# Optimization experiments

Measured on AMD Instinct MI355X. Metric: run time of the kernel, lower is better.

The kernel has to match this reference:

```python
import jax, jax.numpy as jnp
import numpy as np

B, S, D = 2, 2048, 4096
H, KVH, HD = 32, 8, 128
WIN = 1024  # sliding window
THETA = 10000.0


def setup_inputs() -> dict:
    key = jax.random.key(0)
    ks = jax.random.split(key, 5)
    x = jax.random.normal(ks[0], (B, S, D), jnp.float32) * 0.02
    wq = jax.random.normal(ks[1], (H * HD, D), jnp.float32) * 0.02
    wk = jax.random.normal(ks[2], (KVH * HD, D), jnp.float32) * 0.02
    wv = jax.random.normal(ks[3], (KVH * HD, D), jnp.float32) * 0.02
    wo = jax.random.normal(ks[4], (D, H * HD), jnp.float32) * 0.02
    positions = jnp.arange(S, dtype=jnp.int32)
    inv_freq = 1.0 / (THETA ** (jnp.arange(0, HD, 2, dtype=jnp.float32) / HD))
    ang = positions.astype(jnp.float32)[:, None] * inv_freq[None, :]  # [S, HD/2]
    cos, sin = jnp.cos(ang), jnp.sin(ang)
    i = jnp.arange(S)[:, None]
    j = jnp.arange(S)[None, :]
    allowed = (j <= i) & (i - j < WIN)  # causal + sliding window
    mask = jnp.where(allowed, 0.0, -1e9).astype(jnp.float32)  # [S, S]
    return {"x": x, "wq": wq, "wk": wk, "wv": wv, "wo": wo,
            "cos": cos, "sin": sin, "mask": mask, "positions": positions}


def _apply_rope(t, cos, sin):
    # t: [B, S, nH, HD]; pairs are consecutive dims (torch view_as_complex layout)
    tr = t.reshape(t.shape[:-1] + (HD // 2, 2))
    t0, t1 = tr[..., 0], tr[..., 1]
    c = cos[None, :, None, :]
    s = sin[None, :, None, :]
    out = jnp.stack([t0 * c - t1 * s, t0 * s + t1 * c], axis=-1)
    return out.reshape(t.shape)


def reference(x, wq, wk, wv, wo, cos, sin, mask, positions):
    bsz, seqlen, _ = x.shape
    xq = (x @ wq.T).reshape(bsz, seqlen, H, HD)
    xk = (x @ wk.T).reshape(bsz, seqlen, KVH, HD)
    xv = (x @ wv.T).reshape(bsz, seqlen, KVH, HD)
    xq = _apply_rope(xq, cos, sin)
    xk = _apply_rope(xk, cos, sin)
    # GQA: repeat_kv head broadcast (prefill path: positions.size(0) > 1)
    rep = H // KVH
    key = jnp.repeat(xk, rep, axis=2)  # [B, S, H, HD]
    val = jnp.repeat(xv, rep, axis=2)
    q = xq.transpose(0, 2, 1, 3)  # [B, H, S, HD]
    k = key.transpose(0, 2, 1, 3)
    v = val.transpose(0, 2, 1, 3)
    scale = HD ** -0.5
    scores = jnp.einsum("bhqd,bhkd->bhqk", q, k) * scale
    scores = scores + mask[None, None, :, :]
    probs = jax.nn.softmax(scores.astype(jnp.float32), axis=-1).astype(q.dtype)
    out = jnp.einsum("bhqk,bhkd->bhqd", probs, v)
    out = out.transpose(0, 2, 1, 3).reshape(bsz, seqlen, H * HD)
    return out @ wo.T
```

## Files before the change

kernel.cpp:

```cpp
#include <hip/hip_runtime.h>
#include <hip/hip_bf16.h>

#define B_  2
#define S_  2048
#define D_  4096
#define H_  32
#define KVH_ 8
#define HD_ 128
#define WIN_ 1024
#define KVSTR 2048

typedef __attribute__((ext_vector_type(8))) __bf16 bf16x8;
typedef __attribute__((ext_vector_type(4))) float f32x4;
using bf16 = __hip_bfloat16;

typedef const __attribute__((address_space(1))) void* gas_ptr;
typedef __attribute__((address_space(3))) void* las_ptr;

__device__ __forceinline__ void gload16(const void* g, void* l) {
    __builtin_amdgcn_global_load_lds((gas_ptr)g, (las_ptr)l, 16, 0, 0);
}

__device__ __forceinline__ bf16x8 load8(const bf16* p) {
    return *reinterpret_cast<const bf16x8*>(p);
}
__device__ __forceinline__ bf16x8 cvt8(const bf16* p) {
    return *reinterpret_cast<const bf16x8*>(p);
}
__device__ __forceinline__ bf16x8 cvt8(const float* p) {
    const float4* q = reinterpret_cast<const float4*>(p);
    float4 a = q[0], b = q[1];
    bf16x8 r;
    r[0] = (__bf16)a.x; r[1] = (__bf16)a.y; r[2] = (__bf16)a.z; r[3] = (__bf16)a.w;
    r[4] = (__bf16)b.x; r[5] = (__bf16)b.y; r[6] = (__bf16)b.z; r[7] = (__bf16)b.w;
    return r;
}
__device__ __forceinline__ void store1(float* p, float v) { *p = v; }
__device__ __forceinline__ void store1(bf16* p, float v) { *p = __float2bfloat16(v); }

#define GBAR()  __builtin_amdgcn_s_barrier()
#define SCB0()  __builtin_amdgcn_sched_barrier(0)
#define LGKM0() do { asm volatile("s_waitcnt lgkmcnt(0)" ::: "memory"); \
                     __builtin_amdgcn_sched_barrier(0); } while (0)
#define VMC(n)  do { asm volatile("s_waitcnt vmcnt(" #n ")" ::: "memory"); \
                     __builtin_amdgcn_sched_barrier(0); } while (0)

__global__ __launch_bounds__(256) void cast_kernel(const float* __restrict__ in,
                                                   bf16* __restrict__ out) {
    long i = ((long)blockIdx.x * 256 + threadIdx.x) * 8;
    const float4* p = reinterpret_cast<const float4*>(in + i);
    float4 a = p[0], b = p[1];
    bf16x8 r;
    r[0] = (__bf16)a.x; r[1] = (__bf16)a.y; r[2] = (__bf16)a.z; r[3] = (__bf16)a.w;
    r[4] = (__bf16)b.x; r[5] = (__bf16)b.y; r[6] = (__bf16)b.z; r[7] = (__bf16)b.w;
    *reinterpret_cast<bf16x8*>(out + i) = r;
}

__global__ __launch_bounds__(256) void cast2_kernel(
    const float* __restrict__ in0, bf16* __restrict__ out0,
    const float* __restrict__ in1, bf16* __restrict__ out1, int n0blocks) {
    const bool first = (int)blockIdx.x < n0blocks;
    const float* in = first ? in0 : in1;
    bf16* out = first ? out0 : out1;
    long bid = first ? blockIdx.x : (blockIdx.x - n0blocks);
    long i = (bid * 256 + threadIdx.x) * 8;
    const float4* p = reinterpret_cast<const float4*>(in + i);
    float4 a = p[0], b = p[1];
    bf16x8 r;
    r[0] = (__bf16)a.x; r[1] = (__bf16)a.y; r[2] = (__bf16)a.z; r[3] = (__bf16)a.w;
    r[4] = (__bf16)b.x; r[5] = (__bf16)b.y; r[6] = (__bf16)b.z; r[7] = (__bf16)b.w;
    *reinterpret_cast<bf16x8*>(out + i) = r;
}

__device__ __forceinline__ void xcd_swizzle(int& bx, int& by, int nbx, int nby) {
    int flat = bx + nbx * by;
    int nwg  = nbx * nby;
    int cpx  = nwg >> 3;
    int swz  = (flat & 7) * cpx + (flat >> 3);
    bx = swz % nbx;
    by = swz / nbx;
}

template <typename TC>
__global__ __launch_bounds__(512, 2) void gemm_nt_256(
    const bf16* __restrict__ A, const bf16* __restrict__ Bm,
    TC* __restrict__ C, int M, int N, int K) {
    __shared__ __bf16 lds[2][2][256 * 64];

    const int tid  = threadIdx.x;
    const int wave = tid >> 6;
    const int lane = tid & 63;
    const int col  = lane & 15;
    const int quad = lane >> 4;
    const int c7   = col & 7;
    const int wmi  = wave >> 2;
    const int wni  = wave & 3;
    int bx = blockIdx.x, by = blockIdx.y;
    xcd_swizzle(bx, by, gridDim.x, gridDim.y);
    const long m0  = (long)by * 256;
    const long n0  = (long)bx * 256;
    const int  nt  = K >> 6;

    f32x4 zero = {0.f, 0.f, 0.f, 0.f};
    f32x4 acc[8][4];
#pragma unroll
    for (int i = 0; i < 8; i++)
#pragma unroll
        for (int j = 0; j < 4; j++) acc[i][j] = zero;

    long gA[4], gB[4];
    int  lofs[4];
#pragma unroll
    for (int j = 0; j < 4; j++) {
        int r  = j * 64 + wave * 8 + (lane >> 3);
        int cg = (lane & 7) ^ (r & 7);
        gA[j]   = (m0 + r) * (long)K + cg * 8;
        gB[j]   = (n0 + r) * (long)K + cg * 8;
        lofs[j] = (j * 64 + wave * 8) * 128;
    }

#pragma unroll
    for (int j = 0; j < 4; j++) {
        gload16(A  + gA[j], (char*)lds[0][0] + lofs[j]);
        gload16(Bm + gB[j], (char*)lds[0][1] + lofs[j]);
    }
    if (nt > 1) {
#pragma unroll
        for (int j = 0; j < 4; j++)
            gload16(Bm + gB[j] + 64, (char*)lds[1][1] + lofs[j]);
        gload16(A + gA[0] + 64, (char*)lds[1][0] + lofs[0]);
        gload16(A + gA[2] + 64, (char*)lds[1][0] + lofs[2]);
        VMC(6);
    } else {
        VMC(0);
    }
    GBAR();

#define RDA_(dst, mf, ks) \
    dst = *reinterpret_cast<const bf16x8*>(Ab + (wmi * 128 + (mf) * 16 + col) * 128 \
                                              + ((((ks) << 2) + quad) ^ c7) * 16)
#define MFMA16(mb) \
    do { \
        _Pragma("unroll") \
        for (int ks = 0; ks < 2; ks++) { \
            _Pragma("unroll") \
            for (int nf = 0; nf < 4; nf++) { \
                acc[mb][nf]     = __builtin_amdgcn_mfma_f32_16x16x32_bf16( \
                    a[0][ks], bfr[nf][ks], acc[mb][nf], 0, 0, 0); \
                acc[mb + 1][nf] = __builtin_amdgcn_mfma_f32_16x16x32_bf16( \
                    a[1][ks], bfr[nf][ks], acc[mb + 1][nf], 0, 0, 0); \
            } \
        } \
    } while (0)

    for (int t = 0; t < nt; ++t) {
        const int cur = t & 1;
        const char* Ab = (const char*)lds[cur][0];
        const char* Bb = (const char*)lds[cur][1];
        char* An2 = (char*)lds[cur ^ 1][0];
        char* Ac2 = (char*)lds[cur][0];
        char* Bc2 = (char*)lds[cur][1];

        bf16x8 bfr[4][2];
#pragma unroll
        for (int nf = 0; nf < 4; nf++)
#pragma unroll
            for (int ks = 0; ks < 2; ks++)
                bfr[nf][ks] = *reinterpret_cast<const bf16x8*>(
                    Bb + (wni * 64 + nf * 16 + col) * 128 + (((ks << 2) + quad) ^ c7) * 16);
        bf16x8 a[2][2];
        RDA_(a[0][0], 0, 0); RDA_(a[0][1], 0, 1);
        RDA_(a[1][0], 1, 0); RDA_(a[1][1], 1, 1);
        if (t + 1 < nt) {
            long ko = (long)(t + 1) * 64;
            gload16(A + gA[1] + ko, An2 + lofs[1]);
            gload16(A + gA[3] + ko, An2 + lofs[3]);
        }
        GBAR();
        LGKM0();
        __builtin_amdgcn_s_setprio(1);
        MFMA16(0);
        __builtin_amdgcn_s_setprio(0);
        GBAR();

        RDA_(a[0][0], 2, 0); RDA_(a[0][1], 2, 1);
        RDA_(a[1][0], 3, 0); RDA_(a[1][1], 3, 1);
        if (t + 2 < nt) {
            long ko = (long)(t + 2) * 64;
#pragma unroll
            for (int j = 0; j < 4; j++)
                gload16(Bm + gB[j] + ko, Bc2 + lofs[j]);
        }
        GBAR();
        LGKM0();
        __builtin_amdgcn_s_setprio(1);
        MFMA16(2);
        __builtin_amdgcn_s_setprio(0);
        GBAR();

        RDA_(a[0][0], 4, 0); RDA_(a[0][1], 4, 1);
        RDA_(a[1][0], 5, 0); RDA_(a[1][1], 5, 1);
        if (t + 2 < nt) {
            long ko = (long)(t + 2) * 64;
            gload16(A + gA[0] + ko, Ac2 + lofs[0]);
            gload16(A + gA[2] + ko, Ac2 + lofs[2]);
        }
        GBAR();
        LGKM0();
        __builtin_amdgcn_s_setprio(1);
        MFMA16(4);
        __builtin_amdgcn_s_setprio(0);
        GBAR();

        RDA_(a[0][0], 6, 0); RDA_(a[0][1], 6, 1);
        RDA_(a[1][0], 7, 0); RDA_(a[1][1], 7, 1);
        LGKM0();
        __builtin_amdgcn_s_setprio(1);
        MFMA16(6);
        __builtin_amdgcn_s_setprio(0);
        if (t + 2 < nt) { VMC(6); } else { VMC(0); }
        GBAR();
    }

#pragma unroll
    for (int mf = 0; mf < 8; mf++) {
#pragma unroll
        for (int nf = 0; nf < 4; nf++) {
            long row = m0 + wmi * 128 + mf * 16 + quad * 4;
            long cc  = n0 + wni * 64 + nf * 16 + col;
#pragma unroll
            for (int r = 0; r < 4; r++)
                store1(&C[(row + r) * (long)N + cc], acc[mf][nf][r]);
        }
    }
}

template <typename TC>
__global__ __launch_bounds__(256) void gemm_nt_fast(
    const bf16* __restrict__ A, const bf16* __restrict__ Bm,
    TC* __restrict__ C, int M, int N, int K) {
    __shared__ __bf16 As[128 * 64];
    __shared__ __bf16 Bs[128 * 64];

    const int tid  = threadIdx.x;
    const int wave = tid >> 6;
    const int lane = tid & 63;
    const int col  = lane & 15;
    const int quad = lane >> 4;
    const int c7   = col & 7;
    const int wm   = (wave >> 1) * 64;
    const int wn   = (wave & 1) * 64;
    int bx = blockIdx.x, by = blockIdx.y;
    xcd_swizzle(bx, by, gridDim.x, gridDim.y);
    const long m0  = (long)by * 128;
    const long n0  = (long)bx * 128;

    f32x4 zero = {0.f, 0.f, 0.f, 0.f};
    f32x4 acc[4][4];
#pragma unroll
    for (int i = 0; i < 4; i++)
#pragma unroll
        for (int j = 0; j < 4; j++) acc[i][j] = zero;

    long goffA[4], goffB[4];
    int  loff[4];
#pragma unroll
    for (int i = 0; i < 4; i++) {
        int r  = (wave * 4 + i) * 8 + (lane >> 3);
        int cg = (lane & 7) ^ (r & 7);
        goffA[i] = (m0 + r) * (long)K + cg * 8;
        goffB[i] = (n0 + r) * (long)K + cg * 8;
        loff[i]  = (wave * 4 + i) * 1024;
    }

    for (int kt = 0; kt < K; kt += 64) {
#pragma unroll
        for (int i = 0; i < 4; i++) {
            gload16(A + goffA[i] + kt, (char*)As + loff[i]);
            gload16(Bm + goffB[i] + kt, (char*)Bs + loff[i]);
        }
        __syncthreads();

        bf16x8 af[2][4], bfv[2][4];
#pragma unroll
        for (int ks = 0; ks < 2; ks++) {
#pragma unroll
            for (int mt = 0; mt < 4; mt++) {
                int row = wm + mt * 16 + col;
                af[ks][mt] = *reinterpret_cast<const bf16x8*>(
                    (const char*)As + row * 128 + (((ks << 2) + quad) ^ c7) * 16);
            }
#pragma unroll
            for (int nt = 0; nt < 4; nt++) {
                int row = wn + nt * 16 + col;
                bfv[ks][nt] = *reinterpret_cast<const bf16x8*>(
                    (const char*)Bs + row * 128 + (((ks << 2) + quad) ^ c7) * 16);
            }
        }
#pragma unroll
        for (int ks = 0; ks < 2; ks++)
#pragma unroll
            for (int mt = 0; mt < 4; mt++)
#pragma unroll
                for (int nt = 0; nt < 4; nt++)
                    acc[mt][nt] = __builtin_amdgcn_mfma_f32_16x16x32_bf16(
                        af[ks][mt], bfv[ks][nt], acc[mt][nt], 0, 0, 0);
        __syncthreads();
    }

#pragma unroll
    for (int mt = 0; mt < 4; mt++) {
#pragma unroll
        for (int nt = 0; nt < 4; nt++) {
            long row = m0 + wm + mt * 16 + quad * 4;
            long cc  = n0 + wn + nt * 16 + col;
#pragma unroll
            for (int r = 0; r < 4; r++)
                store1(&C[(row + r) * (long)N + cc], acc[mt][nt][r]);
        }
    }
}

template <typename TA, typename TB, typename TC>
__global__ __launch_bounds__(256) void gemm_nt(
    const TA* __restrict__ A, const TB* __restrict__ Bm,
    TC* __restrict__ C, int M, int N, int K, int ldc) {
    __shared__ __bf16 As[128 * 40];
    __shared__ __bf16 Bs[128 * 40];

    const int tid  = threadIdx.x;
    const int wave = tid >> 6;
    const int lane = tid & 63;
    const int col  = lane & 15;
    const int quad = lane >> 4;
    const int wm   = (wave >> 1) * 64;
    const int wn   = (wave & 1) * 64;
    const long m0  = (long)blockIdx.y * 128;
    const long n0  = (long)blockIdx.x * 128;

    f32x4 zero = {0.f, 0.f, 0.f, 0.f};
    f32x4 acc[4][4];
#pragma unroll
    for (int i = 0; i < 4; i++)
#pragma unroll
        for (int j = 0; j < 4; j++) acc[i][j] = zero;

    const int srow = tid >> 2;
    const int sch  = (tid & 3) * 8;

    for (int kt = 0; kt < K; kt += 32) {
        bf16x8 av0 = cvt8(A + (m0 + srow)      * (long)K + kt + sch);
        bf16x8 av1 = cvt8(A + (m0 + srow + 64) * (long)K + kt + sch);
        bf16x8 bv0 = cvt8(Bm + (n0 + srow)      * (long)K + kt + sch);
        bf16x8 bv1 = cvt8(Bm + (n0 + srow + 64) * (long)K + kt + sch);
        *reinterpret_cast<bf16x8*>(&As[srow * 40 + sch])        = av0;
        *reinterpret_cast<bf16x8*>(&As[(srow + 64) * 40 + sch]) = av1;
        *reinterpret_cast<bf16x8*>(&Bs[srow * 40 + sch])        = bv0;
        *reinterpret_cast<bf16x8*>(&Bs[(srow + 64) * 40 + sch]) = bv1;
        __syncthreads();

        bf16x8 af[4], bfv[4];
#pragma unroll
        for (int mt = 0; mt < 4; mt++)
            af[mt] = *reinterpret_cast<const bf16x8*>(&As[(wm + mt * 16 + col) * 40 + quad * 8]);
#pragma unroll
        for (int nt = 0; nt < 4; nt++)
            bfv[nt] = *reinterpret_cast<const bf16x8*>(&Bs[(wn + nt * 16 + col) * 40 + quad * 8]);
#pragma unroll
        for (int mt = 0; mt < 4; mt++)
#pragma unroll
            for (int nt = 0; nt < 4; nt++)
                acc[mt][nt] = __builtin_amdgcn_mfma_f32_16x16x32_bf16(
                    af[mt], bfv[nt], acc[mt][nt], 0, 0, 0);
        __syncthreads();
    }

#pragma unroll
    for (int mt = 0; mt < 4; mt++) {
#pragma unroll
        for (int nt = 0; nt < 4; nt++) {
            long row = m0 + wm + mt * 16 + quad * 4;
            long cc  = n0 + wn + nt * 16 + col;
#pragma unroll
            for (int r = 0; r < 4; r++)
                store1(&C[(row + r) * (long)ldc + cc], acc[mt][nt][r]);
        }
    }
}

__global__ __launch_bounds__(256) void rope2_kernel(
    bf16* __restrict__ qb, bf16* __restrict__ kvb,
    const float* __restrict__ cosb, const float* __restrict__ sinb) {
    const int NQ = B_ * S_ * H_ * 64;
    int idx = blockIdx.x * 256 + threadIdx.x;
    bf16* t; int nh, stride;
    if (idx < NQ) { t = qb;  nh = H_;   stride = H_ * HD_; }
    else          { t = kvb; nh = KVH_; stride = KVSTR; idx -= NQ; }
    int pair = idx & 63;
    int rest = idx >> 6;
    int hh   = rest % nh;
    int tok  = rest / nh;
    int s    = tok & (S_ - 1);
    long base = (long)tok * stride + hh * HD_ + pair * 2;
    float c  = cosb[s * 64 + pair];
    float sn = sinb[s * 64 + pair];
    float t0 = __bfloat162float(t[base]);
    float t1 = __bfloat162float(t[base + 1]);
    t[base]     = __float2bfloat16(t0 * c - t1 * sn);
    t[base + 1] = __float2bfloat16(t0 * sn + t1 * c);
}

__global__ __launch_bounds__(256) void transpose_v(const bf16* __restrict__ kv,
                                                   bf16* __restrict__ vt) {
    __shared__ __bf16 tile[64][72];
    const int s0 = blockIdx.x * 64;
    const int d0 = blockIdx.y * 64;
    const int b  = blockIdx.z;
    const int tid = threadIdx.x;
    const int tr  = tid >> 3;
    const int c8  = (tid & 7) * 8;
#pragma unroll
    for (int p = 0; p < 2; p++) {
        int srow = tr + p * 32;
        bf16x8 val = load8(kv + ((long)(b * S_ + s0 + srow)) * KVSTR + 1024 + d0 + c8);
        *reinterpret_cast<bf16x8*>(&tile[srow][c8]) = val;
    }
    __syncthreads();
#pragma unroll
    for (int p = 0; p < 2; p++) {
        int dd = tr + p * 32;
        bf16x8 ov;
#pragma unroll
        for (int j = 0; j < 8; j++) ov[j] = tile[c8 + j][dd];
        *reinterpret_cast<bf16x8*>(vt + ((long)(b * 1024 + d0 + dd)) * S_ + s0 + c8) = ov;
    }
}

__global__ __launch_bounds__(512, 4) void attn_kernel(
    const bf16* __restrict__ q, const bf16* __restrict__ kv,
    const bf16* __restrict__ vt, bf16* __restrict__ o) {
    const int qb  = blockIdx.x;
    const int hp  = blockIdx.y;
    const int b   = blockIdx.z;
    const int tid = threadIdx.x;
    const int wave = tid >> 6;
    const int lane = tid & 63;
    const int col  = lane & 15;
    const int quad = lane >> 4;
    const int h    = hp * 2 + (wave >> 2);
    const int wq4  = wave & 3;
    const int kvh  = hp >> 1;
    const int i0   = qb * 64;
    const float scale = 0.08838834764831845f;

    __shared__ __bf16 Ks[64 * 128];
    __shared__ __bf16 Vs[128 * 64];
    __shared__ __bf16 Pl[8][16 * 72];

    bf16x8 qa[4];
    const bf16* qptr = q + ((long)(b * S_ + i0 + wq4 * 16 + col)) * (H_ * HD_)
                         + h * HD_ + quad * 8;
#pragma unroll
    for (int ks = 0; ks < 4; ks++) qa[ks] = load8(qptr + ks * 32);

    long gK[2], gV[2];
    int  lK[2], lV[2];
#pragma unroll
    for (int i = 0; i < 2; i++) {
        int ck  = wave * 2 + i;
        int rK  = ck * 4 + (lane >> 4);
        int cgK = (lane & 15) ^ (rK & 15);
        gK[i] = ((long)(b * S_) + rK) * KVSTR + kvh * HD_ + cgK * 8;
        lK[i] = ck * 1024;
        int rV  = ck * 8 + (lane >> 3);
        int cgV = (lane & 7) ^ (rV & 7);
        gV[i] = ((long)(b * 1024) + kvh * HD_ + rV) * (long)S_ + cgV * 8;
        lV[i] = ck * 1024;
    }

    f32x4 zero = {0.f, 0.f, 0.f, 0.f};
    f32x4 oacc[8];
#pragma unroll
    for (int i = 0; i < 8; i++) oacc[i] = zero;
    float lsum[4] = {0.f, 0.f, 0.f, 0.f};

    const int kb0 = (qb >= 16) ? (qb - 16) : 0;

    bf16x8 kreg[2], vreg[2];
#pragma unroll
    for (int i = 0; i < 2; i++) {
        kreg[i] = *reinterpret_cast<const bf16x8*>(kv + gK[i] + (long)kb0 * 64 * KVSTR);
        vreg[i] = *reinterpret_cast<const bf16x8*>(vt + gV[i] + kb0 * 64);
    }

    for (int kb = kb0; kb <= qb; kb++) {
        GBAR();
        SCB0();
#pragma unroll
        for (int i = 0; i < 2; i++) {
            *reinterpret_cast<bf16x8*>((char*)Ks + lK[i] + lane * 16) = kreg[i];
            *reinterpret_cast<bf16x8*>((char*)Vs + lV[i] + lane * 16) = vreg[i];
        }
        LGKM0();
        GBAR();
        SCB0();
        if (kb < qb) {
#pragma unroll
            for (int i = 0; i < 2; i++) {
                kreg[i] = *reinterpret_cast<const bf16x8*>(
                    kv + gK[i] + (long)(kb + 1) * 64 * KVSTR);
                vreg[i] = *reinterpret_cast<const bf16x8*>(
                    vt + gV[i] + (kb + 1) * 64);
            }
            SCB0();
        }

        f32x4 sfr[4];
        __builtin_amdgcn_s_setprio(1);
#pragma unroll
        for (int nt = 0; nt < 4; nt++) {
            f32x4 s = zero;
            int row = nt * 16 + col;
#pragma unroll
            for (int ks = 0; ks < 4; ks++) {
                bf16x8 bfv = *reinterpret_cast<const bf16x8*>(
                    (const char*)Ks + row * 256 + (((ks << 2) + quad) ^ col) * 16);
                s = __builtin_amdgcn_mfma_f32_16x16x32_bf16(qa[ks], bfv, s, 0, 0, 0);
            }
            sfr[nt] = s;
        }
        __builtin_amdgcn_s_setprio(0);
#pragma unroll
        for (int nt = 0; nt < 4; nt++) {
            int j = kb * 64 + nt * 16 + col;
#pragma unroll
            for (int r = 0; r < 4; r++) {
                int i = i0 + wq4 * 16 + quad * 4 + r;
                float p = 0.f;
                if (j <= i && (i - j) < WIN_) p = __expf(sfr[nt][r] * scale);
                lsum[r] += p;
                Pl[wave][(quad * 4 + r) * 72 + nt * 16 + col] = __float2bfloat16(p);
            }
        }
        __builtin_amdgcn_s_setprio(1);
#pragma unroll
        for (int ks2 = 0; ks2 < 2; ks2++) {
            bf16x8 pa = *reinterpret_cast<const bf16x8*>(
                &Pl[wave][col * 72 + ks2 * 32 + quad * 8]);
#pragma unroll
            for (int nt2 = 0; nt2 < 8; nt2++) {
                int d = nt2 * 16 + col;
                bf16x8 vb = *reinterpret_cast<const bf16x8*>(
                    (const char*)Vs + d * 128 + ((((ks2 << 2) + quad)) ^ (col & 7)) * 16);
                oacc[nt2] = __builtin_amdgcn_mfma_f32_16x16x32_bf16(
                    pa, vb, oacc[nt2], 0, 0, 0);
            }
        }
        __builtin_amdgcn_s_setprio(0);
    }

#pragma unroll
    for (int m = 1; m < 16; m <<= 1) {
#pragma unroll
        for (int r = 0; r < 4; r++) lsum[r] += __shfl_xor(lsum[r], m, 64);
    }

    bf16* op = o + ((long)(b * S_ + i0 + wq4 * 16 + quad * 4)) * (H_ * HD_) + h * HD_;
#pragma unroll
    for (int nt2 = 0; nt2 < 8; nt2++) {
#pragma unroll
        for (int r = 0; r < 4; r++)
            op[(long)r * (H_ * HD_) + nt2 * 16 + col] =
                __float2bfloat16(oacc[nt2][r] / lsum[r]);
    }
}

extern "C" void kernel_launch(void* const* d_in, const int* in_sizes, int n_in,
                              void* d_out, int out_size, void* d_ws, size_t ws_size,
                              hipStream_t stream) {
    const float* x    = (const float*)d_in[0];
    const float* wq   = (const float*)d_in[1];
    const float* wk   = (const float*)d_in[2];
    const float* wv   = (const float*)d_in[3];
    const float* wo   = (const float*)d_in[4];
    const float* cosb = (const float*)d_in[5];
    const float* sinb = (const float*)d_in[6];
    float* out = (float*)d_out;

    const size_t T   = (size_t)B_ * S_;
    const size_t SZ_D  = T * (H_ * HD_);
    const size_t SZ_KV = T * (KVH_ * HD_);

    dim3 blk(256);
    const size_t need_fast = (SZ_D * 3 + SZ_KV * 3 + SZ_D) * 2;

    if (ws_size >= need_fast) {
        bf16* xb    = (bf16*)d_ws;
        bf16* wbuf  = xb    + SZ_D;
        bf16* q_ws  = wbuf  + SZ_D;
        bf16* kv_ws = q_ws  + SZ_D;
        bf16* vt_ws = kv_ws + 2 * SZ_KV;
        bf16* ao_ws = vt_ws + SZ_KV;

        cast2_kernel<<<2 * (SZ_D / 2048), blk, 0, stream>>>(x, xb, wq, wbuf,
                                                            (int)(SZ_D / 2048));
        gemm_nt_256<bf16><<<dim3(16, 16), dim3(512), 0, stream>>>(xb, wbuf, q_ws, 4096, 4096, 4096);

        cast2_kernel<<<2 * (SZ_KV / 2048), blk, 0, stream>>>(wk, wbuf, wv, wbuf + SZ_KV,
                                                             (int)(SZ_KV / 2048));
        gemm_nt_fast<bf16><<<dim3(16, 32), blk, 0, stream>>>(xb, wbuf, kv_ws, 4096, 2048, 4096);

        rope2_kernel<<<(B_ * S_ * (H_ + KVH_) * 64) / 256, blk, 0, stream>>>(
            q_ws, kv_ws, cosb, sinb);
        transpose_v<<<dim3(32, 16, 2), blk, 0, stream>>>(kv_ws, vt_ws);

        attn_kernel<<<dim3(32, 16, 2), dim3(512), 0, stream>>>(q_ws, kv_ws, vt_ws, ao_ws);

        cast_kernel<<<SZ_D / 2048, blk, 0, stream>>>(wo, wbuf);
        gemm_nt_256<float><<<dim3(16, 16), dim3(512), 0, stream>>>(ao_ws, wbuf, out, 4096, 4096, 4096);
    } else {
        bf16* q_ws  = (bf16*)d_ws;
        bf16* kv_ws = q_ws  + SZ_D;
        bf16* vt_ws = kv_ws + 2 * SZ_KV;
        bf16* ao_ws = vt_ws + SZ_KV;

        gemm_nt<float, float, bf16><<<dim3(32, 32), blk, 0, stream>>>(x, wq, q_ws, 4096, 4096, 4096, 4096);
        gemm_nt<float, float, bf16><<<dim3(8, 32),  blk, 0, stream>>>(x, wk, kv_ws, 4096, 1024, 4096, KVSTR);
        gemm_nt<float, float, bf16><<<dim3(8, 32),  blk, 0, stream>>>(x, wv, kv_ws + 1024, 4096, 1024, 4096, KVSTR);

        rope2_kernel<<<(B_ * S_ * (H_ + KVH_) * 64) / 256, blk, 0, stream>>>(
            q_ws, kv_ws, cosb, sinb);
        transpose_v<<<dim3(32, 16, 2), blk, 0, stream>>>(kv_ws, vt_ws);

        attn_kernel<<<dim3(32, 16, 2), dim3(512), 0, stream>>>(q_ws, kv_ws, vt_ws, ao_ws);

        gemm_nt<bf16, float, float><<<dim3(32, 32), blk, 0, stream>>>(ao_ws, wo, out, 4096, 4096, 4096, 4096);
    }
}
```

Baseline: 672.1 us.

## Restructure GEMM MFMA phases by k-slice and double-buffer attention KV register prefetch

```diff
diff --git a/kernel.cpp b/kernel.cpp
--- a/kernel.cpp
+++ b/kernel.cpp
@@ -136,20 +136,26 @@
     }
     GBAR();
 
-#define RDA_(dst, mf, ks) \
-    dst = *reinterpret_cast<const bf16x8*>(Ab + (wmi * 128 + (mf) * 16 + col) * 128 \
-                                              + ((((ks) << 2) + quad) ^ c7) * 16)
-#define MFMA16(mb) \
+#define RD_A(mf, ks) \
+    (*reinterpret_cast<const bf16x8*>(Ab + (wmi * 128 + (mf) * 16 + col) * 128 \
+                                         + ((((ks) << 2) + quad) ^ c7) * 16))
+#define RD_B(nf, ks) \
+    (*reinterpret_cast<const bf16x8*>(Bb + (wni * 64 + (nf) * 16 + col) * 128 \
+                                         + ((((ks) << 2) + quad) ^ c7) * 16))
+#define RDA_G(g, ks) do { \
+    a4[0] = RD_A((g) * 4 + 0, ks); a4[1] = RD_A((g) * 4 + 1, ks); \
+    a4[2] = RD_A((g) * 4 + 2, ks); a4[3] = RD_A((g) * 4 + 3, ks); } while (0)
+#define RDB_K(dst, ks) do { \
+    dst[0] = RD_B(0, ks); dst[1] = RD_B(1, ks); \
+    dst[2] = RD_B(2, ks); dst[3] = RD_B(3, ks); } while (0)
+#define MFMA16G(g, bk) \
     do { \
         _Pragma("unroll") \
-        for (int ks = 0; ks < 2; ks++) { \
+        for (int nf = 0; nf < 4; nf++) { \
             _Pragma("unroll") \
-            for (int nf = 0; nf < 4; nf++) { \
-                acc[mb][nf]     = __builtin_amdgcn_mfma_f32_16x16x32_bf16( \
-                    a[0][ks], bfr[nf][ks], acc[mb][nf], 0, 0, 0); \
-                acc[mb + 1][nf] = __builtin_amdgcn_mfma_f32_16x16x32_bf16( \
-                    a[1][ks], bfr[nf][ks], acc[mb + 1][nf], 0, 0, 0); \
-            } \
+            for (int m = 0; m < 4; m++) \
+                acc[(g) * 4 + m][nf] = __builtin_amdgcn_mfma_f32_16x16x32_bf16( \
+                    a4[m], bk[nf], acc[(g) * 4 + m][nf], 0, 0, 0); \
         } \
     } while (0)
 
@@ -161,16 +167,10 @@
         char* Ac2 = (char*)lds[cur][0];
         char* Bc2 = (char*)lds[cur][1];
 
-        bf16x8 bfr[4][2];
-#pragma unroll
-        for (int nf = 0; nf < 4; nf++)
-#pragma unroll
-            for (int ks = 0; ks < 2; ks++)
-                bfr[nf][ks] = *reinterpret_cast<const bf16x8*>(
-                    Bb + (wni * 64 + nf * 16 + col) * 128 + (((ks << 2) + quad) ^ c7) * 16);
-        bf16x8 a[2][2];
-        RDA_(a[0][0], 0, 0); RDA_(a[0][1], 0, 1);
-        RDA_(a[1][0], 1, 0); RDA_(a[1][1], 1, 1);
+        bf16x8 b0[4], b1[4], a4[4];
+
+        RDB_K(b0, 0);
+        RDA_G(0, 0);
         if (t + 1 < nt) {
             long ko = (long)(t + 1) * 64;
             gload16(A + gA[1] + ko, An2 + lofs[1]);
@@ -179,12 +179,20 @@
         GBAR();
         LGKM0();
         __builtin_amdgcn_s_setprio(1);
-        MFMA16(0);
+        MFMA16G(0, b0);
         __builtin_amdgcn_s_setprio(0);
         GBAR();
 
-        RDA_(a[0][0], 2, 0); RDA_(a[0][1], 2, 1);
-        RDA_(a[1][0], 3, 0); RDA_(a[1][1], 3, 1);
+        RDA_G(1, 0);
+        RDB_K(b1, 1);
+        GBAR();
+        LGKM0();
+        __builtin_amdgcn_s_setprio(1);
+        MFMA16G(1, b0);
+        __builtin_amdgcn_s_setprio(0);
+        GBAR();
+
+        RDA_G(0, 1);
         if (t + 2 < nt) {
             long ko = (long)(t + 2) * 64;
 #pragma unroll
@@ -194,12 +202,11 @@
         GBAR();
         LGKM0();
         __builtin_amdgcn_s_setprio(1);
-        MFMA16(2);
+        MFMA16G(0, b1);
         __builtin_amdgcn_s_setprio(0);
         GBAR();
 
-        RDA_(a[0][0], 4, 0); RDA_(a[0][1], 4, 1);
-        RDA_(a[1][0], 5, 0); RDA_(a[1][1], 5, 1);
+        RDA_G(1, 1);
         if (t + 2 < nt) {
             long ko = (long)(t + 2) * 64;
             gload16(A + gA[0] + ko, Ac2 + lofs[0]);
@@ -208,15 +215,7 @@
         GBAR();
         LGKM0();
         __builtin_amdgcn_s_setprio(1);
-        MFMA16(4);
-        __builtin_amdgcn_s_setprio(0);
-        GBAR();
-
-        RDA_(a[0][0], 6, 0); RDA_(a[0][1], 6, 1);
-        RDA_(a[1][0], 7, 0); RDA_(a[1][1], 7, 1);
-        LGKM0();
-        __builtin_amdgcn_s_setprio(1);
-        MFMA16(6);
+        MFMA16G(1, b1);
         __builtin_amdgcn_s_setprio(0);
         if (t + 2 < nt) { VMC(6); } else { VMC(0); }
         GBAR();
@@ -478,6 +477,15 @@
         lV[i] = ck * 1024;
     }
 
+#define STAGE_LOAD(kr, vr, kbn) \
+    do { _Pragma("unroll") for (int i = 0; i < 2; i++) { \
+        kr[i] = *reinterpret_cast<const bf16x8*>(kv + gK[i] + (long)(kbn) * 64 * KVSTR); \
+        vr[i] = *reinterpret_cast<const bf16x8*>(vt + gV[i] + (kbn) * 64); } } while (0)
+#define STAGE_WRITE(kr, vr) \
+    do { _Pragma("unroll") for (int i = 0; i < 2; i++) { \
+        *reinterpret_cast<bf16x8*>((char*)Ks + lK[i] + lane * 16) = kr[i]; \
+        *reinterpret_cast<bf16x8*>((char*)Vs + lV[i] + lane * 16) = vr[i]; } } while (0)
+
     f32x4 zero = {0.f, 0.f, 0.f, 0.f};
     f32x4 oacc[8];
 #pragma unroll
@@ -486,32 +494,21 @@
 
     const int kb0 = (qb >= 16) ? (qb - 16) : 0;
 
-    bf16x8 kreg[2], vreg[2];
-#pragma unroll
-    for (int i = 0; i < 2; i++) {
-        kreg[i] = *reinterpret_cast<const bf16x8*>(kv + gK[i] + (long)kb0 * 64 * KVSTR);
-        vreg[i] = *reinterpret_cast<const bf16x8*>(vt + gV[i] + kb0 * 64);
-    }
+    bf16x8 kA[2], vA[2], kB[2], vB[2];
+    STAGE_LOAD(kA, vA, kb0);
+    if (kb0 + 1 <= qb) STAGE_LOAD(kB, vB, kb0 + 1);
 
     for (int kb = kb0; kb <= qb; kb++) {
+        const bool useA = ((kb - kb0) & 1) == 0;
         GBAR();
         SCB0();
-#pragma unroll
-        for (int i = 0; i < 2; i++) {
-            *reinterpret_cast<bf16x8*>((char*)Ks + lK[i] + lane * 16) = kreg[i];
-            *reinterpret_cast<bf16x8*>((char*)Vs + lV[i] + lane * 16) = vreg[i];
-        }
+        if (useA) STAGE_WRITE(kA, vA); else STAGE_WRITE(kB, vB);
         LGKM0();
         GBAR();
         SCB0();
-        if (kb < qb) {
-#pragma unroll
-            for (int i = 0; i < 2; i++) {
-                kreg[i] = *reinterpret_cast<const bf16x8*>(
-                    kv + gK[i] + (long)(kb + 1) * 64 * KVSTR);
-                vreg[i] = *reinterpret_cast<const bf16x8*>(
-                    vt + gV[i] + (kb + 1) * 64);
-            }
+        if (kb + 2 <= qb) {
+            if (useA) STAGE_LOAD(kA, vA, kb + 2);
+            else      STAGE_LOAD(kB, vB, kb + 2);
             SCB0();
         }
 
```

New measurement: 697.6 us. 3.8% more time.
